# Kernel tuning notes

Hardware: AMD Instinct MI355X
Metric: run time of the kernel (lower is better)

## Reference

```python
import jax, jax.numpy as jnp
import numpy as np

ARITY = 2
DEPTH = 11          # full tree: levels 0..DEPTH, leaves at DEPTH
H = 1024
V = 32001           # vocab_size + 1 (null token)


def _preorder_perm(depth, arity):
    """Permutation mapping pre-order position -> BFS (level-concatenated) index."""
    offsets = np.concatenate([[0], np.cumsum(arity ** np.arange(depth + 1))])
    order = []
    def rec(d, p):
        order.append(int(offsets[d] + p))
        if d < depth:
            for c in range(arity):
                rec(d + 1, p * arity + c)
    rec(0, 0)
    return np.asarray(order, dtype=np.int32)

_PERM = _preorder_perm(DEPTH, ARITY)


def setup_inputs() -> dict:
    key = jax.random.key(0)
    ks = jax.random.split(key, 9)
    s = 0.02  # small init scale for numerical sanity
    return {
        "root_hidden": jax.random.normal(ks[0], (H,), jnp.float32),
        "W1v": jax.random.normal(ks[1], (H, 2 * H), jnp.float32) * s,
        "b1v": jax.random.normal(ks[2], (2 * H,), jnp.float32) * s,
        "W2v": jax.random.normal(ks[3], (2 * H, V), jnp.float32) * s,
        "b2v": jax.random.normal(ks[4], (V,), jnp.float32) * s,
        "W1c": jax.random.normal(ks[5], (H, 2 * H), jnp.float32) * s,
        "b1c": jax.random.normal(ks[6], (2 * H,), jnp.float32) * s,
        "W2c": jax.random.normal(ks[7], (2 * H, ARITY * H), jnp.float32) * s,
        "b2c": jax.random.normal(ks[8], (ARITY * H,), jnp.float32) * s,
    }


def _mlp(h, W1, b1, W2, b2):
    # Linear -> Sigmoid -> Linear (matches nn.Sequential in the torch module)
    return jax.nn.sigmoid(h @ W1 + b1) @ W2 + b2


def reference(root_hidden, W1v, b1v, W2v, b2v, W1c, b1c, W2c, b2c):
    # Level-wise vectorized sweep over the full tree (batches all nodes at a depth).
    h = root_hidden[None, :]                  # [1, H]
    prods = []
    for d in range(DEPTH + 1):
        prods.append(_mlp(h, W1v, b1v, W2v, b2v))     # [a^d, V]
        if d < DEPTH:
            # to_children then split into arity children per node
            h = _mlp(h, W1c, b1c, W2c, b2c).reshape(-1, H)  # [a^(d+1), H]
    raw = jnp.concatenate(prods, axis=0)      # BFS order, [N, V]
    raw = raw[_PERM]                          # reorder to pre-order (torch recursion order)
    return jax.nn.log_softmax(raw, axis=1)
```

## Files before the change

kernel.cpp:

```cpp
#include <hip/hip_runtime.h>
#include <hip/hip_bf16.h>

#define DEPTH_T 11
#define HDIM 1024
#define VDIM 32001
#define NNODES 4095
#define LDV 32008

typedef __attribute__((ext_vector_type(8))) short bf16x8;
typedef __attribute__((ext_vector_type(8))) unsigned short ushort8;
typedef __attribute__((ext_vector_type(4))) float floatx4;

__device__ __forceinline__ int preorder_pos(int m) {
    int q = m + 1;
    int d = 31 - __clz(q);
    int pos = 0;
    for (int i = 1; i <= d; ++i) {
        int b = (q >> (d - i)) & 1;
        pos += 1 + b * ((1 << (DEPTH_T - i + 1)) - 1);
    }
    return pos;
}

__device__ __forceinline__ float bf2f(unsigned short u) {
    return __uint_as_float(((unsigned)u) << 16);
}

#define BM 128
#define BN 128
#define BK 32

template<int MODE, bool SWAPG>
__global__ __launch_bounds__(256, 2) void gemm_bt(
    const __hip_bfloat16* __restrict__ A,
    const __hip_bfloat16* __restrict__ Bt,
    const float* __restrict__ bias,
    void* __restrict__ outp,
    int M, int N, int K, int ldout)
{
    __shared__ __align__(16) __hip_bfloat16 As[BM][BK];
    __shared__ __align__(16) __hip_bfloat16 Bs[BN][BK];

    const int tid  = threadIdx.x;
    const int wave = tid >> 6;
    const int lane = tid & 63;
    const int m0 = (SWAPG ? blockIdx.x : blockIdx.y) * BM;
    const int n0 = (SWAPG ? blockIdx.y : blockIdx.x) * BN;
    const int wm = (wave & 1) * 64;
    const int wn = (wave >> 1) * 64;

    floatx4 acc[4][4];
#pragma unroll
    for (int i = 0; i < 4; ++i)
#pragma unroll
        for (int j = 0; j < 4; ++j) acc[i][j] = (floatx4)0.0f;

    const int lrow = lane >> 2;
    const int lcol = (lane & 3) * 8;
    const int fr = lane & 15;
    const int fk = (lane >> 4) * 8;

    for (int k0 = 0; k0 < K; k0 += BK) {
        __syncthreads();
#pragma unroll
        for (int t = 0; t < 2; ++t) {
            const int r = (wave * 2 + t) * 16;
            int gm = m0 + r + lrow; gm = gm < M ? gm : M - 1;
            const __hip_bfloat16* gp = A + (size_t)gm * K + (k0 + lcol);
            __builtin_amdgcn_global_load_lds(
                (const __attribute__((address_space(1))) void*)gp,
                (__attribute__((address_space(3))) void*)(&As[r][0]),
                16, 0, 0);
        }
#pragma unroll
        for (int t = 0; t < 2; ++t) {
            const int r = (wave * 2 + t) * 16;
            int gn = n0 + r + lrow; gn = gn < N ? gn : N - 1;
            const __hip_bfloat16* gp = Bt + (size_t)gn * K + (k0 + lcol);
            __builtin_amdgcn_global_load_lds(
                (const __attribute__((address_space(1))) void*)gp,
                (__attribute__((address_space(3))) void*)(&Bs[r][0]),
                16, 0, 0);
        }
        __syncthreads();

        bf16x8 af[4], bfv[4];
#pragma unroll
        for (int i = 0; i < 4; ++i)
            af[i] = *(const bf16x8*)(&As[wm + i * 16 + fr][fk]);
#pragma unroll
        for (int j = 0; j < 4; ++j)
            bfv[j] = *(const bf16x8*)(&Bs[wn + j * 16 + fr][fk]);
#pragma unroll
        for (int i = 0; i < 4; ++i)
#pragma unroll
            for (int j = 0; j < 4; ++j)
                acc[i][j] = __builtin_amdgcn_mfma_f32_16x16x32_bf16(
                    af[i], bfv[j], acc[i][j], 0, 0, 0);
    }

    const int rq = (lane >> 4) * 4;
    if (MODE >= 2) {
#pragma unroll
        for (int i = 0; i < 4; ++i) {
#pragma unroll
            for (int r = 0; r < 4; ++r) {
                const int gm = m0 + wm + i * 16 + rq + r;
                if (gm >= M) continue;
                const size_t orow = (size_t)preorder_pos(gm) * ldout;
#pragma unroll
                for (int j = 0; j < 4; ++j) {
                    const int gn = n0 + wn + j * 16 + fr;
                    if (gn < N) {
                        float v = acc[i][j][r] + bias[gn];
                        if (MODE == 2) ((float*)outp)[orow + gn] = v;
                        else ((__hip_bfloat16*)outp)[orow + gn] = __float2bfloat16(v);
                    }
                }
            }
        }
    } else {
        __hip_bfloat16* O = (__hip_bfloat16*)outp;
#pragma unroll
        for (int i = 0; i < 4; ++i) {
#pragma unroll
            for (int r = 0; r < 4; ++r) {
                const int gm = m0 + wm + i * 16 + rq + r;
                if (gm >= M) continue;
#pragma unroll
                for (int j = 0; j < 4; ++j) {
                    const int gn = n0 + wn + j * 16 + fr;
                    if (gn < N) {
                        float v = acc[i][j][r] + bias[gn];
                        if (MODE == 0) v = 1.0f / (1.0f + __expf(-v));
                        O[(size_t)gm * ldout + gn] = __float2bfloat16(v);
                    }
                }
            }
        }
    }
}

#define B2M 256
#define B2N 256

template<int MODE>
__global__ __launch_bounds__(512, 2) void gemm256(
    const __hip_bfloat16* __restrict__ A,
    const __hip_bfloat16* __restrict__ Bt,
    const float* __restrict__ bias,
    void* __restrict__ outp,
    int M, int N, int K, int ldout)
{
    __shared__ __align__(16) char smem[131072];

    const int tid  = threadIdx.x;
    const int wave = tid >> 6;
    const int lane = tid & 63;

    const int nwy = (N + B2N - 1) / B2N;
    int mt, nt;
    {
        const int g = blockIdx.x >> 8;
        const int i = blockIdx.x & 255;
        const int k = i & 7, s = i >> 3;
        mt = (k & 1) * 4 + (s & 3) + (g & 1) * 8;
        nt = (k >> 1) * 8 + (s >> 2) + (g >> 1) * 32;
    }
    if (nt >= nwy) return;
    const int m0 = mt * B2M;
    const int n0 = nt * B2N;

    const int wm = (wave >> 2) * 128;
    const int wn = (wave & 3) * 64;
    const int nkt = K >> 6;

    const int s_row = lane >> 3;
    const int s_col = ((lane & 7) ^ s_row) * 8;

    const int fr  = lane & 15;
    const int fkq = lane >> 4;
    const int swz = (fr & 7) << 4;
    const int c0  = (fkq * 16) ^ swz;
    const int c1  = (64 + fkq * 16) ^ swz;
    const int aoff = (wm + fr) * 128;
    const int boff = 32768 + (wn + fr) * 128;

    floatx4 acc[8][4];
#pragma unroll
    for (int i = 0; i < 8; ++i)
#pragma unroll
        for (int j = 0; j < 4; ++j) acc[i][j] = (floatx4)0.0f;

    bf16x8 a0[8], a1[8], b0[4], b1[4];

    auto mkb = [&](const __hip_bfloat16* gb, int g0, int lim, int h, int inst) {
        int gr = g0 + h * 128 + (inst * 8 + wave) * 8 + s_row;
        gr = gr < lim ? gr : lim - 1;
        return gb + (size_t)gr * K + s_col;
    };
    const __hip_bfloat16* pA00 = mkb(A,  m0, M, 0, 0);
    const __hip_bfloat16* pA01 = mkb(A,  m0, M, 0, 1);
    const __hip_bfloat16* pA10 = mkb(A,  m0, M, 1, 0);
    const __hip_bfloat16* pA11 = mkb(A,  m0, M, 1, 1);
    const __hip_bfloat16* pB00 = mkb(Bt, n0, N, 0, 0);
    const __hip_bfloat16* pB01 = mkb(Bt, n0, N, 0, 1);
    const __hip_bfloat16* pB10 = mkb(Bt, n0, N, 1, 0);
    const __hip_bfloat16* pB11 = mkb(Bt, n0, N, 1, 1);

#define STAGE(bsel, mat, h, PP0, PP1, kt) do { \
    const int ko_ = ((kt) < nkt ? (kt) : 0) * 64; \
    __builtin_amdgcn_global_load_lds( \
        (const __attribute__((address_space(1))) void*)((PP0) + ko_), \
        (__attribute__((address_space(3))) void*) \
            (smem + (bsel)*65536 + (mat)*32768 + (h)*16384 + wave*1024), 16, 0, 0); \
    __builtin_amdgcn_global_load_lds( \
        (const __attribute__((address_space(1))) void*)((PP1) + ko_), \
        (__attribute__((address_space(3))) void*) \
            (smem + (bsel)*65536 + (mat)*32768 + (h)*16384 + 8192 + wave*1024), 16, 0, 0); \
} while (0)

#define RD_A(dst, bsel, cc) \
    _Pragma("unroll") \
    for (int i = 0; i < 8; ++i) \
        dst[i] = *(const bf16x8*)(smem + (bsel) * 65536 + aoff + i * 2048 + (cc));
#define RD_B(dst, bsel, cc) \
    _Pragma("unroll") \
    for (int j = 0; j < 4; ++j) \
        dst[j] = *(const bf16x8*)(smem + (bsel) * 65536 + boff + j * 2048 + (cc));
#define MM(ib, AA, BB) \
    _Pragma("unroll") \
    for (int i = 0; i < 4; ++i) \
    _Pragma("unroll") \
    for (int j = 0; j < 4; ++j) \
        acc[(ib) + i][j] = __builtin_amdgcn_mfma_f32_16x16x32_bf16( \
            AA[(ib) + i], BB[j], acc[(ib) + i][j], 0, 0, 0);
#define LGKM0  asm volatile("s_waitcnt lgkmcnt(0)" ::: "memory")
#define VM4    asm volatile("s_waitcnt vmcnt(4)" ::: "memory")
#define BAR    __builtin_amdgcn_s_barrier()
#define PRIO1  __builtin_amdgcn_s_setprio(1)
#define PRIO0  __builtin_amdgcn_s_setprio(0)

    STAGE(0, 0, 0, pA00, pA01, 0);
    STAGE(0, 0, 1, pA10, pA11, 0);
    STAGE(0, 1, 0, pB00, pB01, 0);
    STAGE(0, 1, 1, pB10, pB11, 0);
    STAGE(1, 0, 0, pA00, pA01, 1);
    STAGE(1, 0, 1, pA10, pA11, 1);
    VM4;
    BAR;

#pragma unroll 1
    for (int t = 0; t < nkt; t += 2) {
        RD_A(a0, 0, c0); RD_B(b0, 0, c0);
        STAGE(1, 1, 0, pB00, pB01, t + 1);
        BAR; LGKM0;
        PRIO1; MM(0, a0, b0); PRIO0;
        BAR;
        RD_A(a1, 0, c1); RD_B(b1, 0, c1);
        STAGE(1, 1, 1, pB10, pB11, t + 1);
        BAR; LGKM0;
        PRIO1; MM(4, a0, b0); PRIO0;
        BAR;
        STAGE(0, 0, 0, pA00, pA01, t + 2);
        BAR;
        PRIO1; MM(0, a1, b1); PRIO0;
        BAR;
        STAGE(0, 0, 1, pA10, pA11, t + 2);
        VM4;
        BAR;
        PRIO1; MM(4, a1, b1); PRIO0;
        BAR;
        RD_A(a0, 1, c0); RD_B(b0, 1, c0);
        STAGE(0, 1, 0, pB00, pB01, t + 2);
        BAR; LGKM0;
        PRIO1; MM(0, a0, b0); PRIO0;
        BAR;
        RD_A(a1, 1, c1); RD_B(b1, 1, c1);
        STAGE(0, 1, 1, pB10, pB11, t + 2);
        BAR; LGKM0;
        PRIO1; MM(4, a0, b0); PRIO0;
        BAR;
        STAGE(1, 0, 0, pA00, pA01, t + 3);
        BAR;
        PRIO1; MM(0, a1, b1); PRIO0;
        BAR;
        STAGE(1, 0, 1, pA10, pA11, t + 3);
        VM4;
        BAR;
        PRIO1; MM(4, a1, b1); PRIO0;
        BAR;
    }

#undef STAGE
#undef RD_A
#undef RD_B
#undef MM
#undef LGKM0
#undef VM4
#undef BAR
#undef PRIO1
#undef PRIO0

    const int rq = (lane >> 4) * 4;
    if (MODE >= 2) {
#pragma unroll
        for (int i = 0; i < 8; ++i) {
#pragma unroll
            for (int r = 0; r < 4; ++r) {
                const int gm = m0 + wm + i * 16 + rq + r;
                if (gm >= M) continue;
                const size_t orow = (size_t)preorder_pos(gm) * ldout;
#pragma unroll
                for (int j = 0; j < 4; ++j) {
                    const int gn = n0 + wn + j * 16 + fr;
                    if (gn < N) {
                        float v = acc[i][j][r] + bias[gn];
                        if (MODE == 2) ((float*)outp)[orow + gn] = v;
                        else ((__hip_bfloat16*)outp)[orow + gn] = __float2bfloat16(v);
                    }
                }
            }
        }
    } else {
        __hip_bfloat16* O = (__hip_bfloat16*)outp;
#pragma unroll
        for (int i = 0; i < 8; ++i) {
#pragma unroll
            for (int r = 0; r < 4; ++r) {
                const int gm = m0 + wm + i * 16 + rq + r;
                if (gm >= M) continue;
#pragma unroll
                for (int j = 0; j < 4; ++j) {
                    const int gn = n0 + wn + j * 16 + fr;
                    if (gn < N) {
                        float v = acc[i][j][r] + bias[gn];
                        if (MODE == 0) v = 1.0f / (1.0f + __expf(-v));
                        O[(size_t)gm * ldout + gn] = __float2bfloat16(v);
                    }
                }
            }
        }
    }
}

template<int MODE>
__global__ __launch_bounds__(256) void gemm_small(
    const __hip_bfloat16* __restrict__ A,
    const __hip_bfloat16* __restrict__ Bt,
    const float* __restrict__ bias,
    __hip_bfloat16* __restrict__ O,
    int M, int N, int K)
{
    const int wave = threadIdx.x >> 6, lane = threadIdx.x & 63;
    const int n0 = blockIdx.x * 64 + wave * 16;
    const int m0 = blockIdx.y * 16;
    const int fr = lane & 15, fk = (lane >> 4) * 8;

    int am = m0 + fr; am = am < M ? am : M - 1;
    const __hip_bfloat16* ap = A + (size_t)am * K + fk;
    const __hip_bfloat16* bp = Bt + (size_t)(n0 + fr) * K + fk;

    floatx4 acc = (floatx4)0.0f;
#pragma unroll 8
    for (int k0 = 0; k0 < K; k0 += 32) {
        bf16x8 av = *(const bf16x8*)(ap + k0);
        bf16x8 bv = *(const bf16x8*)(bp + k0);
        acc = __builtin_amdgcn_mfma_f32_16x16x32_bf16(av, bv, acc, 0, 0, 0);
    }

    const int rq = (lane >> 4) * 4;
    const int gn = n0 + fr;
    const float b = bias[gn];
#pragma unroll
    for (int r = 0; r < 4; ++r) {
        const int gm = m0 + rq + r;
        if (gm >= M) continue;
        float v = acc[r] + b;
        if (MODE == 0) v = 1.0f / (1.0f + __expf(-v));
        O[(size_t)gm * N + gn] = __float2bfloat16(v);
    }
}

__global__ __launch_bounds__(256) void transpose_to_bf16(
    const float* __restrict__ in, __hip_bfloat16* __restrict__ outT, int R, int C)
{
    __shared__ float tile[64][65];
    const int c0 = blockIdx.x * 64, r0 = blockIdx.y * 64;
    const int tx = threadIdx.x & 63, ty = threadIdx.x >> 6;
#pragma unroll
    for (int i = 0; i < 64; i += 4) {
        int r = r0 + ty + i, c = c0 + tx;
        tile[ty + i][tx] = (r < R && c < C) ? in[(size_t)r * C + c] : 0.0f;
    }
    __syncthreads();
#pragma unroll
    for (int i = 0; i < 64; i += 4) {
        int rr = c0 + ty + i, cc = r0 + tx;
        if (rr < C && cc < R) outT[(size_t)rr * R + cc] = __float2bfloat16(tile[tx][ty + i]);
    }
}

__global__ __launch_bounds__(256) void convert_root(
    const float* __restrict__ in, __hip_bfloat16* __restrict__ out)
{
    int i = blockIdx.x * 256 + threadIdx.x;
    if (i < HDIM) out[i] = __float2bfloat16(in[i]);
}

__global__ __launch_bounds__(256) void logsoftmax_bf16(
    const unsigned short* __restrict__ L, float* __restrict__ O)
{
    extern __shared__ char smem[];
    unsigned short* rb = (unsigned short*)smem;
    float* wred = (float*)(smem + 64016);
    const int tid = threadIdx.x, lane = tid & 63, wv = tid >> 6;
    const unsigned short* src = L + (size_t)blockIdx.x * LDV;

    float m = -3.0e38f;
    for (int j = tid * 8; j < 32000; j += 2048) {
        ushort8 u = *(const ushort8*)(src + j);
        *(ushort8*)(rb + j) = u;
#pragma unroll
        for (int t = 0; t < 8; ++t) m = fmaxf(m, bf2f(u[t]));
    }
    if (tid == 0) { unsigned short u = src[32000]; rb[32000] = u; m = fmaxf(m, bf2f(u)); }
#pragma unroll
    for (int off = 32; off; off >>= 1) m = fmaxf(m, __shfl_xor(m, off, 64));
    if (lane == 0) wred[wv] = m;
    __syncthreads();
    const float M4 = fmaxf(fmaxf(wred[0], wred[1]), fmaxf(wred[2], wred[3]));

    float s = 0.0f;
    for (int j = tid * 8; j < 32000; j += 2048) {
        ushort8 u = *(const ushort8*)(rb + j);
#pragma unroll
        for (int t = 0; t < 8; ++t) s += __expf(bf2f(u[t]) - M4);
    }
    if (tid == 0) s += __expf(bf2f(rb[32000]) - M4);
#pragma unroll
    for (int off = 32; off; off >>= 1) s += __shfl_xor(s, off, 64);
    if (lane == 0) wred[4 + wv] = s;
    __syncthreads();
    const float lse = M4 + __logf(wred[4] + wred[5] + wred[6] + wred[7]);

    float* dst = O + (size_t)blockIdx.x * VDIM;
    for (int j = tid * 8; j < 32000; j += 2048) {
        ushort8 u = *(const ushort8*)(rb + j);
#pragma unroll
        for (int t = 0; t < 8; ++t) dst[j + t] = bf2f(u[t]) - lse;
    }
    if (tid == 0) dst[32000] = bf2f(rb[32000]) - lse;
}

__global__ __launch_bounds__(256) void logsoftmax_rows(float* __restrict__ O, int n)
{
    __shared__ float sm[256], ssum[256];
    const int tid = threadIdx.x;
    float* p = O + (size_t)blockIdx.x * n;
    float m = -3.0e38f, s = 0.0f;
    for (int j = tid; j < n; j += 256) {
        float x = p[j];
        float nm = fmaxf(m, x);
        s = s * __expf(m - nm) + __expf(x - nm);
        m = nm;
    }
    sm[tid] = m; ssum[tid] = s;
    __syncthreads();
    for (int off = 128; off > 0; off >>= 1) {
        if (tid < off) {
            float m2 = sm[tid + off], s2 = ssum[tid + off];
            float nm = fmaxf(sm[tid], m2);
            ssum[tid] = ssum[tid] * __expf(sm[tid] - nm) + s2 * __expf(m2 - nm);
            sm[tid] = nm;
        }
        __syncthreads();
    }
    const float lse = sm[0] + __logf(ssum[0]);
    for (int j = tid; j < n; j += 256) p[j] -= lse;
}

extern "C" void kernel_launch(void* const* d_in, const int* in_sizes, int n_in,
                              void* d_out, int out_size, void* d_ws, size_t ws_size,
                              hipStream_t stream)
{
    const float* root = (const float*)d_in[0];
    const float* W1v  = (const float*)d_in[1];
    const float* b1v  = (const float*)d_in[2];
    const float* W2v  = (const float*)d_in[3];
    const float* b2v  = (const float*)d_in[4];
    const float* W1c  = (const float*)d_in[5];
    const float* b1c  = (const float*)d_in[6];
    const float* W2c  = (const float*)d_in[7];
    const float* b2c  = (const float*)d_in[8];

    char* ws = (char*)d_ws;
    __hip_bfloat16* Hall = (__hip_bfloat16*)(ws + 0);
    __hip_bfloat16* X1   = (__hip_bfloat16*)(ws +   8388608ull);
    __hip_bfloat16* Tt   = (__hip_bfloat16*)(ws +  25165824ull);
    __hip_bfloat16* W1vT = (__hip_bfloat16*)(ws +  29360128ull);
    __hip_bfloat16* W1cT = (__hip_bfloat16*)(ws +  33554432ull);
    __hip_bfloat16* W2cT = (__hip_bfloat16*)(ws +  37748736ull);
    __hip_bfloat16* W2vT = (__hip_bfloat16*)(ws +  46137344ull);
    __hip_bfloat16* Lb   = (__hip_bfloat16*)(ws + 177213440ull);
    const bool bf16_logits = ws_size >= 177213440ull + (size_t)NNODES * LDV * 2;

    dim3 blk(256);

    transpose_to_bf16<<<dim3( 32, 16), blk, 0, stream>>>(W1v, W1vT, 1024, 2048);
    transpose_to_bf16<<<dim3(501, 32), blk, 0, stream>>>(W2v, W2vT, 2048, VDIM);
    transpose_to_bf16<<<dim3( 32, 16), blk, 0, stream>>>(W1c, W1cT, 1024, 2048);
    transpose_to_bf16<<<dim3( 32, 32), blk, 0, stream>>>(W2c, W2cT, 2048, 2048);
    convert_root<<<dim3(4), blk, 0, stream>>>(root, Hall);

    for (int d = 0; d < DEPTH_T; ++d) {
        const int Md = 1 << d;
        __hip_bfloat16* Hd = Hall + (size_t)(Md - 1) * HDIM;
        __hip_bfloat16* Hn = Hall + (size_t)((2 << d) - 1) * HDIM;
        if (Md <= 256) {
            dim3 g(32, (Md + 15) / 16);
            gemm_small<0><<<g, blk, 0, stream>>>(Hd, W1cT, b1c, Tt, Md, 2048, 1024);
            gemm_small<1><<<g, blk, 0, stream>>>(Tt, W2cT, b2c, Hn, Md, 2048, 2048);
        } else {
            dim3 g(16, Md / 128);
            gemm_bt<0, false><<<g, blk, 0, stream>>>(Hd, W1cT, b1c, Tt, Md, 2048, 1024, 2048);
            gemm_bt<1, false><<<g, blk, 0, stream>>>(Tt, W2cT, b2c, Hn, Md, 2048, 2048, 2048);
        }
    }

    gemm_bt<0, false><<<dim3(16, 32), blk, 0, stream>>>(Hall, W1vT, b1v, X1, NNODES, 2048, 1024, 2048);
    if (bf16_logits) {
        gemm256<3><<<dim3(2048), dim3(512), 0, stream>>>(X1, W2vT, b2v, Lb, NNODES, VDIM, 2048, LDV);
        logsoftmax_bf16<<<dim3(NNODES), blk, 64048, stream>>>((const unsigned short*)Lb, (float*)d_out);
    } else {
        gemm_bt<2, true><<<dim3(32, 251), blk, 0, stream>>>(X1, W2vT, b2v, d_out, NNODES, VDIM, 2048, VDIM);
        logsoftmax_rows<<<dim3(NNODES), blk, 0, stream>>>((float*)d_out, VDIM);
    }
}
```

Measured before the change: 1.440 ms.

## Run vocab projection GEMM in FP8 e4m3 with FP8 weight transpose and activations

The large vocab GEMM (4095x32001x2048) moves from bf16 MFMA to fp8 e4m3 MFMA. The W2v transpose now writes fp8, and the first vocab MLP layer emits its sigmoid activations directly as fp8. The main kernel's LDS staging is halved and re-swizzled for byte-sized elements, and its register fragments become 64-bit longs. The aim is to double MFMA throughput and halve operand bandwidth for the dominant GEMM, at the cost of much lower precision in the logits, which may break the accuracy tolerance.

After: 1.610 ms. 11.8% more time.

```diff
diff --git a/kernel.cpp b/kernel.cpp
--- a/kernel.cpp
+++ b/kernel.cpp
@@ -24,6 +24,10 @@
 
 __device__ __forceinline__ float bf2f(unsigned short u) {
     return __uint_as_float(((unsigned)u) << 16);
+}
+
+__device__ __forceinline__ unsigned char f2e4m3(float v) {
+    return (unsigned char)(__builtin_amdgcn_cvt_pk_fp8_f32(v, v, 0, false) & 0xff);
 }
 
 #define BM 128
@@ -100,7 +104,7 @@
     }
 
     const int rq = (lane >> 4) * 4;
-    if (MODE >= 2) {
+    if (MODE == 2 || MODE == 3) {
 #pragma unroll
         for (int i = 0; i < 4; ++i) {
 #pragma unroll
@@ -120,7 +124,6 @@
             }
         }
     } else {
-        __hip_bfloat16* O = (__hip_bfloat16*)outp;
 #pragma unroll
         for (int i = 0; i < 4; ++i) {
 #pragma unroll
@@ -132,8 +135,11 @@
                     const int gn = n0 + wn + j * 16 + fr;
                     if (gn < N) {
                         float v = acc[i][j][r] + bias[gn];
-                        if (MODE == 0) v = 1.0f / (1.0f + __expf(-v));
-                        O[(size_t)gm * ldout + gn] = __float2bfloat16(v);
+                        if (MODE != 1) v = 1.0f / (1.0f + __expf(-v));
+                        if (MODE == 4)
+                            ((unsigned char*)outp)[(size_t)gm * ldout + gn] = f2e4m3(v);
+                        else
+                            ((__hip_bfloat16*)outp)[(size_t)gm * ldout + gn] = __float2bfloat16(v);
                     }
                 }
             }
@@ -144,15 +150,14 @@
 #define B2M 256
 #define B2N 256
 
-template<int MODE>
-__global__ __launch_bounds__(512, 2) void gemm256(
-    const __hip_bfloat16* __restrict__ A,
-    const __hip_bfloat16* __restrict__ Bt,
+__global__ __launch_bounds__(512, 1) void gemm256_f8(
+    const unsigned char* __restrict__ A,
+    const unsigned char* __restrict__ Bt,
     const float* __restrict__ bias,
-    void* __restrict__ outp,
+    __hip_bfloat16* __restrict__ outp,
     int M, int N, int K, int ldout)
 {
-    __shared__ __align__(16) char smem[131072];
+    __shared__ __align__(16) char smem[65536];
 
     const int tid  = threadIdx.x;
     const int wave = tid >> 6;
@@ -175,16 +180,16 @@
     const int wn = (wave & 3) * 64;
     const int nkt = K >> 6;
 
-    const int s_row = lane >> 3;
-    const int s_col = ((lane & 7) ^ s_row) * 8;
+    const int s_row = tid >> 2;
+    const int s_col = ((tid & 3) * 16) ^ ((s_row & 3) << 4);
 
     const int fr  = lane & 15;
     const int fkq = lane >> 4;
-    const int swz = (fr & 7) << 4;
-    const int c0  = (fkq * 16) ^ swz;
-    const int c1  = (64 + fkq * 16) ^ swz;
-    const int aoff = (wm + fr) * 128;
-    const int boff = 32768 + (wn + fr) * 128;
+    const int sw  = (fr & 3) << 4;
+    const int c0  = (fkq * 8) ^ sw;
+    const int c1  = (32 + fkq * 8) ^ sw;
+    const int aoff = (wm + fr) * 64;
+    const int boff = 16384 + (wn + fr) * 64;
 
     floatx4 acc[8][4];
 #pragma unroll
@@ -192,152 +197,122 @@
 #pragma unroll
         for (int j = 0; j < 4; ++j) acc[i][j] = (floatx4)0.0f;
 
-    bf16x8 a0[8], a1[8], b0[4], b1[4];
-
-    auto mkb = [&](const __hip_bfloat16* gb, int g0, int lim, int h, int inst) {
-        int gr = g0 + h * 128 + (inst * 8 + wave) * 8 + s_row;
+    long a0[8], a1[8], b0[4], b1[4];
+
+    auto mkb = [&](const unsigned char* gb, int g0, int lim, int h) {
+        int gr = g0 + h * 128 + s_row;
         gr = gr < lim ? gr : lim - 1;
         return gb + (size_t)gr * K + s_col;
     };
-    const __hip_bfloat16* pA00 = mkb(A,  m0, M, 0, 0);
-    const __hip_bfloat16* pA01 = mkb(A,  m0, M, 0, 1);
-    const __hip_bfloat16* pA10 = mkb(A,  m0, M, 1, 0);
-    const __hip_bfloat16* pA11 = mkb(A,  m0, M, 1, 1);
-    const __hip_bfloat16* pB00 = mkb(Bt, n0, N, 0, 0);
-    const __hip_bfloat16* pB01 = mkb(Bt, n0, N, 0, 1);
-    const __hip_bfloat16* pB10 = mkb(Bt, n0, N, 1, 0);
-    const __hip_bfloat16* pB11 = mkb(Bt, n0, N, 1, 1);
-
-#define STAGE(bsel, mat, h, PP0, PP1, kt) do { \
+    const unsigned char* pAlo = mkb(A,  m0, M, 0);
+    const unsigned char* pAhi = mkb(A,  m0, M, 1);
+    const unsigned char* pBlo = mkb(Bt, n0, N, 0);
+    const unsigned char* pBhi = mkb(Bt, n0, N, 1);
+
+#define STAGE8(bsel, mat, h, PP, kt) do { \
     const int ko_ = ((kt) < nkt ? (kt) : 0) * 64; \
     __builtin_amdgcn_global_load_lds( \
-        (const __attribute__((address_space(1))) void*)((PP0) + ko_), \
+        (const __attribute__((address_space(1))) void*)((PP) + ko_), \
         (__attribute__((address_space(3))) void*) \
-            (smem + (bsel)*65536 + (mat)*32768 + (h)*16384 + wave*1024), 16, 0, 0); \
-    __builtin_amdgcn_global_load_lds( \
-        (const __attribute__((address_space(1))) void*)((PP1) + ko_), \
-        (__attribute__((address_space(3))) void*) \
-            (smem + (bsel)*65536 + (mat)*32768 + (h)*16384 + 8192 + wave*1024), 16, 0, 0); \
+            (smem + (bsel)*32768 + (mat)*16384 + (h)*8192 + tid*16), 16, 0, 0); \
 } while (0)
 
-#define RD_A(dst, bsel, cc) \
+#define RD_A8(dst, bsel, cc) \
     _Pragma("unroll") \
     for (int i = 0; i < 8; ++i) \
-        dst[i] = *(const bf16x8*)(smem + (bsel) * 65536 + aoff + i * 2048 + (cc));
-#define RD_B(dst, bsel, cc) \
+        dst[i] = *(const long*)(smem + (bsel) * 32768 + aoff + i * 1024 + (cc));
+#define RD_B8(dst, bsel, cc) \
     _Pragma("unroll") \
     for (int j = 0; j < 4; ++j) \
-        dst[j] = *(const bf16x8*)(smem + (bsel) * 65536 + boff + j * 2048 + (cc));
-#define MM(ib, AA, BB) \
+        dst[j] = *(const long*)(smem + (bsel) * 32768 + boff + j * 1024 + (cc));
+#define MM8(ib, AA, BB) \
     _Pragma("unroll") \
     for (int i = 0; i < 4; ++i) \
     _Pragma("unroll") \
     for (int j = 0; j < 4; ++j) \
-        acc[(ib) + i][j] = __builtin_amdgcn_mfma_f32_16x16x32_bf16( \
+        acc[(ib) + i][j] = __builtin_amdgcn_mfma_f32_16x16x32_fp8_fp8( \
             AA[(ib) + i], BB[j], acc[(ib) + i][j], 0, 0, 0);
 #define LGKM0  asm volatile("s_waitcnt lgkmcnt(0)" ::: "memory")
-#define VM4    asm volatile("s_waitcnt vmcnt(4)" ::: "memory")
+#define VM2    asm volatile("s_waitcnt vmcnt(2)" ::: "memory")
 #define BAR    __builtin_amdgcn_s_barrier()
 #define PRIO1  __builtin_amdgcn_s_setprio(1)
 #define PRIO0  __builtin_amdgcn_s_setprio(0)
 
-    STAGE(0, 0, 0, pA00, pA01, 0);
-    STAGE(0, 0, 1, pA10, pA11, 0);
-    STAGE(0, 1, 0, pB00, pB01, 0);
-    STAGE(0, 1, 1, pB10, pB11, 0);
-    STAGE(1, 0, 0, pA00, pA01, 1);
-    STAGE(1, 0, 1, pA10, pA11, 1);
-    VM4;
+    STAGE8(0, 0, 0, pAlo, 0);
+    STAGE8(0, 0, 1, pAhi, 0);
+    STAGE8(0, 1, 0, pBlo, 0);
+    STAGE8(0, 1, 1, pBhi, 0);
+    STAGE8(1, 0, 0, pAlo, 1);
+    STAGE8(1, 0, 1, pAhi, 1);
+    VM2;
     BAR;
 
 #pragma unroll 1
     for (int t = 0; t < nkt; t += 2) {
-        RD_A(a0, 0, c0); RD_B(b0, 0, c0);
-        STAGE(1, 1, 0, pB00, pB01, t + 1);
+        RD_A8(a0, 0, c0); RD_B8(b0, 0, c0);
+        STAGE8(1, 1, 0, pBlo, t + 1);
         BAR; LGKM0;
-        PRIO1; MM(0, a0, b0); PRIO0;
-        BAR;
-        RD_A(a1, 0, c1); RD_B(b1, 0, c1);
-        STAGE(1, 1, 1, pB10, pB11, t + 1);
+        PRIO1; MM8(0, a0, b0); PRIO0;
+        BAR;
+        RD_A8(a1, 0, c1); RD_B8(b1, 0, c1);
+        STAGE8(1, 1, 1, pBhi, t + 1);
         BAR; LGKM0;
-        PRIO1; MM(4, a0, b0); PRIO0;
-        BAR;
-        STAGE(0, 0, 0, pA00, pA01, t + 2);
-        BAR;
-        PRIO1; MM(0, a1, b1); PRIO0;
-        BAR;
-        STAGE(0, 0, 1, pA10, pA11, t + 2);
-        VM4;
-        BAR;
-        PRIO1; MM(4, a1, b1); PRIO0;
-        BAR;
-        RD_A(a0, 1, c0); RD_B(b0, 1, c0);
-        STAGE(0, 1, 0, pB00, pB01, t + 2);
+        PRIO1; MM8(4, a0, b0); PRIO0;
+        BAR;
+        STAGE8(0, 0, 0, pAlo, t + 2);
+        BAR;
+        PRIO1; MM8(0, a1, b1); PRIO0;
+        BAR;
+        STAGE8(0, 0, 1, pAhi, t + 2);
+        VM2;
+        BAR;
+        PRIO1; MM8(4, a1, b1); PRIO0;
+        BAR;
+        RD_A8(a0, 1, c0); RD_B8(b0, 1, c0);
+        STAGE8(0, 1, 0, pBlo, t + 2);
         BAR; LGKM0;
-        PRIO1; MM(0, a0, b0); PRIO0;
-        BAR;
-        RD_A(a1, 1, c1); RD_B(b1, 1, c1);
-        STAGE(0, 1, 1, pB10, pB11, t + 2);
+        PRIO1; MM8(0, a0, b0); PRIO0;
+        BAR;
+        RD_A8(a1, 1, c1); RD_B8(b1, 1, c1);
+        STAGE8(0, 1, 1, pBhi, t + 2);
         BAR; LGKM0;
-        PRIO1; MM(4, a0, b0); PRIO0;
-        BAR;
-        STAGE(1, 0, 0, pA00, pA01, t + 3);
-        BAR;
-        PRIO1; MM(0, a1, b1); PRIO0;
-        BAR;
-        STAGE(1, 0, 1, pA10, pA11, t + 3);
-        VM4;
-        BAR;
-        PRIO1; MM(4, a1, b1); PRIO0;
-        BAR;
-    }
-
-#undef STAGE
-#undef RD_A
-#undef RD_B
-#undef MM
+        PRIO1; MM8(4, a0, b0); PRIO0;
+        BAR;
+        STAGE8(1, 0, 0, pAlo, t + 3);
+        BAR;
+        PRIO1; MM8(0, a1, b1); PRIO0;
+        BAR;
+        STAGE8(1, 0, 1, pAhi, t + 3);
+        VM2;
+        BAR;
+        PRIO1; MM8(4, a1, b1); PRIO0;
+        BAR;
+    }
+
+#undef STAGE8
+#undef RD_A8
+#undef RD_B8
+#undef MM8
 #undef LGKM0
-#undef VM4
+#undef VM2
 #undef BAR
 #undef PRIO1
 #undef PRIO0
 
     const int rq = (lane >> 4) * 4;
-    if (MODE >= 2) {
-#pragma unroll
-        for (int i = 0; i < 8; ++i) {
-#pragma unroll
-            for (int r = 0; r < 4; ++r) {
-                const int gm = m0 + wm + i * 16 + rq + r;
-                if (gm >= M) continue;
-                const size_t orow = (size_t)preorder_pos(gm) * ldout;
-#pragma unroll
-                for (int j = 0; j < 4; ++j) {
-                    const int gn = n0 + wn + j * 16 + fr;
-                    if (gn < N) {
-                        float v = acc[i][j][r] + bias[gn];
-                        if (MODE == 2) ((float*)outp)[orow + gn] = v;
-                        else ((__hip_bfloat16*)outp)[orow + gn] = __float2bfloat16(v);
-                    }
-                }
-            }
-        }
-    } else {
-        __hip_bfloat16* O = (__hip_bfloat16*)outp;
-#pragma unroll
-        for (int i = 0; i < 8; ++i) {
-#pragma unroll
-            for (int r = 0; r < 4; ++r) {
-                const int gm = m0 + wm + i * 16 + rq + r;
-                if (gm >= M) continue;
-#pragma unroll
-                for (int j = 0; j < 4; ++j) {
-                    const int gn = n0 + wn + j * 16 + fr;
-                    if (gn < N) {
-                        float v = acc[i][j][r] + bias[gn];
-                        if (MODE == 0) v = 1.0f / (1.0f + __expf(-v));
-                        O[(size_t)gm * ldout + gn] = __float2bfloat16(v);
-                    }
+#pragma unroll
+    for (int i = 0; i < 8; ++i) {
+#pragma unroll
+        for (int r = 0; r < 4; ++r) {
+            const int gm = m0 + wm + i * 16 + rq + r;
+            if (gm >= M) continue;
+            const size_t orow = (size_t)preorder_pos(gm) * ldout;
+#pragma unroll
+            for (int j = 0; j < 4; ++j) {
+                const int gn = n0 + wn + j * 16 + fr;
+                if (gn < N) {
+                    float v = acc[i][j][r] + bias[gn];
+                    outp[orow + gn] = __float2bfloat16(v);
                 }
             }
         }
@@ -398,6 +373,25 @@
     for (int i = 0; i < 64; i += 4) {
         int rr = c0 + ty + i, cc = r0 + tx;
         if (rr < C && cc < R) outT[(size_t)rr * R + cc] = __float2bfloat16(tile[tx][ty + i]);
+    }
+}
+
+__global__ __launch_bounds__(256) void transpose_to_fp8(
+    const float* __restrict__ in, unsigned char* __restrict__ outT, int R, int C)
+{
+    __shared__ float tile[64][65];
+    const int c0 = blockIdx.x * 64, r0 = blockIdx.y * 64;
+    const int tx = threadIdx.x & 63, ty = threadIdx.x >> 6;
+#pragma unroll
+    for (int i = 0; i < 64; i += 4) {
+        int r = r0 + ty + i, c = c0 + tx;
+        tile[ty + i][tx] = (r < R && c < C) ? in[(size_t)r * C + c] : 0.0f;
+    }
+    __syncthreads();
+#pragma unroll
+    for (int i = 0; i < 64; i += 4) {
+        int rr = c0 + ty + i, cc = r0 + tx;
+        if (rr < C && cc < R) outT[(size_t)rr * R + cc] = f2e4m3(tile[tx][ty + i]);
     }
 }
 
@@ -497,18 +491,23 @@
     char* ws = (char*)d_ws;
     __hip_bfloat16* Hall = (__hip_bfloat16*)(ws + 0);
     __hip_bfloat16* X1   = (__hip_bfloat16*)(ws +   8388608ull);
+    unsigned char*  X1_8 = (unsigned char*)(ws +   8388608ull);
     __hip_bfloat16* Tt   = (__hip_bfloat16*)(ws +  25165824ull);
     __hip_bfloat16* W1vT = (__hip_bfloat16*)(ws +  29360128ull);
     __hip_bfloat16* W1cT = (__hip_bfloat16*)(ws +  33554432ull);
     __hip_bfloat16* W2cT = (__hip_bfloat16*)(ws +  37748736ull);
     __hip_bfloat16* W2vT = (__hip_bfloat16*)(ws +  46137344ull);
+    unsigned char*  W2vT8= (unsigned char*)(ws +  46137344ull);
     __hip_bfloat16* Lb   = (__hip_bfloat16*)(ws + 177213440ull);
     const bool bf16_logits = ws_size >= 177213440ull + (size_t)NNODES * LDV * 2;
 
     dim3 blk(256);
 
     transpose_to_bf16<<<dim3( 32, 16), blk, 0, stream>>>(W1v, W1vT, 1024, 2048);
-    transpose_to_bf16<<<dim3(501, 32), blk, 0, stream>>>(W2v, W2vT, 2048, VDIM);
+    if (bf16_logits)
+        transpose_to_fp8<<<dim3(501, 32), blk, 0, stream>>>(W2v, W2vT8, 2048, VDIM);
+    else
+        transpose_to_bf16<<<dim3(501, 32), blk, 0, stream>>>(W2v, W2vT, 2048, VDIM);
     transpose_to_bf16<<<dim3( 32, 16), blk, 0, stream>>>(W1c, W1cT, 1024, 2048);
     transpose_to_bf16<<<dim3( 32, 32), blk, 0, stream>>>(W2c, W2cT, 2048, 2048);
     convert_root<<<dim3(4), blk, 0, stream>>>(root, Hall);
@@ -528,11 +527,12 @@
         }
     }
 
-    gemm_bt<0, false><<<dim3(16, 32), blk, 0, stream>>>(Hall, W1vT, b1v, X1, NNODES, 2048, 1024, 2048);
     if (bf16_logits) {
-        gemm256<3><<<dim3(2048), dim3(512), 0, stream>>>(X1, W2vT, b2v, Lb, NNODES, VDIM, 2048, LDV);
+        gemm_bt<4, false><<<dim3(16, 32), blk, 0, stream>>>(Hall, W1vT, b1v, X1_8, NNODES, 2048, 1024, 2048);
+        gemm256_f8<<<dim3(2048), dim3(512), 0, stream>>>(X1_8, W2vT8, b2v, Lb, NNODES, VDIM, 2048, LDV);
         logsoftmax_bf16<<<dim3(NNODES), blk, 64048, stream>>>((const unsigned short*)Lb, (float*)d_out);
     } else {
+        gemm_bt<0, false><<<dim3(16, 32), blk, 0, stream>>>(Hall, W1vT, b1v, X1, NNODES, 2048, 1024, 2048);
         gemm_bt<2, true><<<dim3(32, 251), blk, 0, stream>>>(X1, W2vT, b2v, d_out, NNODES, VDIM, 2048, VDIM);
         logsoftmax_rows<<<dim3(NNODES), blk, 0, stream>>>((float*)d_out, VDIM);
     }
```

## Run vocab projection GEMM in FP8 e4m3 with FP8 MFMA

Applied to the files above, without the earlier changes.

The big logits GEMM (4095x32001x2048) now takes FP8 e4m3 inputs. W2v is transposed straight to FP8, and the sigmoid hidden layer writes FP8 output. The 256x256 kernel is adapted to 128-wide K steps of bytes and issues two fp8 16x16x32 MFMAs per fragment. This halves operand bandwidth and LDS traffic and uses the higher FP8 MFMA throughput, at the cost of lower precision in the logits.

Measured after the change: 1.366 ms. -5.2%, faster.

```diff
diff --git a/kernel.cpp b/kernel.cpp
--- a/kernel.cpp
+++ b/kernel.cpp
@@ -10,6 +10,7 @@
 typedef __attribute__((ext_vector_type(8))) short bf16x8;
 typedef __attribute__((ext_vector_type(8))) unsigned short ushort8;
 typedef __attribute__((ext_vector_type(4))) float floatx4;
+typedef __attribute__((ext_vector_type(2))) long longx2;
 
 __device__ __forceinline__ int preorder_pos(int m) {
     int q = m + 1;
@@ -24,6 +25,10 @@
 
 __device__ __forceinline__ float bf2f(unsigned short u) {
     return __uint_as_float(((unsigned)u) << 16);
+}
+
+__device__ __forceinline__ unsigned char f2e4m3(float v) {
+    return (unsigned char)(__builtin_amdgcn_cvt_pk_fp8_f32(v, v, 0, false) & 0xff);
 }
 
 #define BM 128
@@ -100,7 +105,7 @@
     }
 
     const int rq = (lane >> 4) * 4;
-    if (MODE >= 2) {
+    if (MODE == 2 || MODE == 3) {
 #pragma unroll
         for (int i = 0; i < 4; ++i) {
 #pragma unroll
@@ -120,7 +125,6 @@
             }
         }
     } else {
-        __hip_bfloat16* O = (__hip_bfloat16*)outp;
 #pragma unroll
         for (int i = 0; i < 4; ++i) {
 #pragma unroll
@@ -132,8 +136,11 @@
                     const int gn = n0 + wn + j * 16 + fr;
                     if (gn < N) {
                         float v = acc[i][j][r] + bias[gn];
-                        if (MODE == 0) v = 1.0f / (1.0f + __expf(-v));
-                        O[(size_t)gm * ldout + gn] = __float2bfloat16(v);
+                        if (MODE != 1) v = 1.0f / (1.0f + __expf(-v));
+                        if (MODE == 4)
+                            ((unsigned char*)outp)[(size_t)gm * ldout + gn] = f2e4m3(v);
+                        else
+                            ((__hip_bfloat16*)outp)[(size_t)gm * ldout + gn] = __float2bfloat16(v);
                     }
                 }
             }
@@ -144,12 +151,11 @@
 #define B2M 256
 #define B2N 256
 
-template<int MODE>
-__global__ __launch_bounds__(512, 2) void gemm256(
-    const __hip_bfloat16* __restrict__ A,
-    const __hip_bfloat16* __restrict__ Bt,
+__global__ __launch_bounds__(512, 2) void gemm256_f8(
+    const unsigned char* __restrict__ A,
+    const unsigned char* __restrict__ Bt,
     const float* __restrict__ bias,
-    void* __restrict__ outp,
+    __hip_bfloat16* __restrict__ outp,
     int M, int N, int K, int ldout)
 {
     __shared__ __align__(16) char smem[131072];
@@ -173,10 +179,10 @@
 
     const int wm = (wave >> 2) * 128;
     const int wn = (wave & 3) * 64;
-    const int nkt = K >> 6;
+    const int nkt = K >> 7;
 
     const int s_row = lane >> 3;
-    const int s_col = ((lane & 7) ^ s_row) * 8;
+    const int s_col = ((lane & 7) ^ s_row) * 16;
 
     const int fr  = lane & 15;
     const int fkq = lane >> 4;
@@ -192,24 +198,24 @@
 #pragma unroll
         for (int j = 0; j < 4; ++j) acc[i][j] = (floatx4)0.0f;
 
-    bf16x8 a0[8], a1[8], b0[4], b1[4];
-
-    auto mkb = [&](const __hip_bfloat16* gb, int g0, int lim, int h, int inst) {
+    longx2 a0[8], a1[8], b0[4], b1[4];
+
+    auto mkb = [&](const unsigned char* gb, int g0, int lim, int h, int inst) {
         int gr = g0 + h * 128 + (inst * 8 + wave) * 8 + s_row;
         gr = gr < lim ? gr : lim - 1;
         return gb + (size_t)gr * K + s_col;
     };
-    const __hip_bfloat16* pA00 = mkb(A,  m0, M, 0, 0);
-    const __hip_bfloat16* pA01 = mkb(A,  m0, M, 0, 1);
-    const __hip_bfloat16* pA10 = mkb(A,  m0, M, 1, 0);
-    const __hip_bfloat16* pA11 = mkb(A,  m0, M, 1, 1);
-    const __hip_bfloat16* pB00 = mkb(Bt, n0, N, 0, 0);
-    const __hip_bfloat16* pB01 = mkb(Bt, n0, N, 0, 1);
-    const __hip_bfloat16* pB10 = mkb(Bt, n0, N, 1, 0);
-    const __hip_bfloat16* pB11 = mkb(Bt, n0, N, 1, 1);
+    const unsigned char* pA00 = mkb(A,  m0, M, 0, 0);
+    const unsigned char* pA01 = mkb(A,  m0, M, 0, 1);
+    const unsigned char* pA10 = mkb(A,  m0, M, 1, 0);
+    const unsigned char* pA11 = mkb(A,  m0, M, 1, 1);
+    const unsigned char* pB00 = mkb(Bt, n0, N, 0, 0);
+    const unsigned char* pB01 = mkb(Bt, n0, N, 0, 1);
+    const unsigned char* pB10 = mkb(Bt, n0, N, 1, 0);
+    const unsigned char* pB11 = mkb(Bt, n0, N, 1, 1);
 
 #define STAGE(bsel, mat, h, PP0, PP1, kt) do { \
-    const int ko_ = ((kt) < nkt ? (kt) : 0) * 64; \
+    const int ko_ = ((kt) < nkt ? (kt) : 0) * 128; \
     __builtin_amdgcn_global_load_lds( \
         (const __attribute__((address_space(1))) void*)((PP0) + ko_), \
         (__attribute__((address_space(3))) void*) \
@@ -223,18 +229,21 @@
 #define RD_A(dst, bsel, cc) \
     _Pragma("unroll") \
     for (int i = 0; i < 8; ++i) \
-        dst[i] = *(const bf16x8*)(smem + (bsel) * 65536 + aoff + i * 2048 + (cc));
+        dst[i] = *(const longx2*)(smem + (bsel) * 65536 + aoff + i * 2048 + (cc));
 #define RD_B(dst, bsel, cc) \
     _Pragma("unroll") \
     for (int j = 0; j < 4; ++j) \
-        dst[j] = *(const bf16x8*)(smem + (bsel) * 65536 + boff + j * 2048 + (cc));
+        dst[j] = *(const longx2*)(smem + (bsel) * 65536 + boff + j * 2048 + (cc));
 #define MM(ib, AA, BB) \
     _Pragma("unroll") \
     for (int i = 0; i < 4; ++i) \
     _Pragma("unroll") \
-    for (int j = 0; j < 4; ++j) \
-        acc[(ib) + i][j] = __builtin_amdgcn_mfma_f32_16x16x32_bf16( \
-            AA[(ib) + i], BB[j], acc[(ib) + i][j], 0, 0, 0);
+    for (int j = 0; j < 4; ++j) { \
+        acc[(ib) + i][j] = __builtin_amdgcn_mfma_f32_16x16x32_fp8_fp8( \
+            AA[(ib) + i][0], BB[j][0], acc[(ib) + i][j], 0, 0, 0); \
+        acc[(ib) + i][j] = __builtin_amdgcn_mfma_f32_16x16x32_fp8_fp8( \
+            AA[(ib) + i][1], BB[j][1], acc[(ib) + i][j], 0, 0, 0); \
+    }
 #define LGKM0  asm volatile("s_waitcnt lgkmcnt(0)" ::: "memory")
 #define VM4    asm volatile("s_waitcnt vmcnt(4)" ::: "memory")
 #define BAR    __builtin_amdgcn_s_barrier()
@@ -303,41 +312,19 @@
 #undef PRIO0
 
     const int rq = (lane >> 4) * 4;
-    if (MODE >= 2) {
-#pragma unroll
-        for (int i = 0; i < 8; ++i) {
-#pragma unroll
-            for (int r = 0; r < 4; ++r) {
-                const int gm = m0 + wm + i * 16 + rq + r;
-                if (gm >= M) continue;
-                const size_t orow = (size_t)preorder_pos(gm) * ldout;
-#pragma unroll
-                for (int j = 0; j < 4; ++j) {
-                    const int gn = n0 + wn + j * 16 + fr;
-                    if (gn < N) {
-                        float v = acc[i][j][r] + bias[gn];
-                        if (MODE == 2) ((float*)outp)[orow + gn] = v;
-                        else ((__hip_bfloat16*)outp)[orow + gn] = __float2bfloat16(v);
-                    }
-                }
-            }
-        }
-    } else {
-        __hip_bfloat16* O = (__hip_bfloat16*)outp;
-#pragma unroll
-        for (int i = 0; i < 8; ++i) {
-#pragma unroll
-            for (int r = 0; r < 4; ++r) {
-                const int gm = m0 + wm + i * 16 + rq + r;
-                if (gm >= M) continue;
-#pragma unroll
-                for (int j = 0; j < 4; ++j) {
-                    const int gn = n0 + wn + j * 16 + fr;
-                    if (gn < N) {
-                        float v = acc[i][j][r] + bias[gn];
-                        if (MODE == 0) v = 1.0f / (1.0f + __expf(-v));
-                        O[(size_t)gm * ldout + gn] = __float2bfloat16(v);
-                    }
+#pragma unroll
+    for (int i = 0; i < 8; ++i) {
+#pragma unroll
+        for (int r = 0; r < 4; ++r) {
+            const int gm = m0 + wm + i * 16 + rq + r;
+            if (gm >= M) continue;
+            const size_t orow = (size_t)preorder_pos(gm) * ldout;
+#pragma unroll
+            for (int j = 0; j < 4; ++j) {
+                const int gn = n0 + wn + j * 16 + fr;
+                if (gn < N) {
+                    float v = acc[i][j][r] + bias[gn];
+                    outp[orow + gn] = __float2bfloat16(v);
                 }
             }
         }
@@ -398,6 +385,25 @@
     for (int i = 0; i < 64; i += 4) {
         int rr = c0 + ty + i, cc = r0 + tx;
         if (rr < C && cc < R) outT[(size_t)rr * R + cc] = __float2bfloat16(tile[tx][ty + i]);
+    }
+}
+
+__global__ __launch_bounds__(256) void transpose_to_fp8(
+    const float* __restrict__ in, unsigned char* __restrict__ outT, int R, int C)
+{
+    __shared__ float tile[64][65];
+    const int c0 = blockIdx.x * 64, r0 = blockIdx.y * 64;
+    const int tx = threadIdx.x & 63, ty = threadIdx.x >> 6;
+#pragma unroll
+    for (int i = 0; i < 64; i += 4) {
+        int r = r0 + ty + i, c = c0 + tx;
+        tile[ty + i][tx] = (r < R && c < C) ? in[(size_t)r * C + c] : 0.0f;
+    }
+    __syncthreads();
+#pragma unroll
+    for (int i = 0; i < 64; i += 4) {
+        int rr = c0 + ty + i, cc = r0 + tx;
+        if (rr < C && cc < R) outT[(size_t)rr * R + cc] = f2e4m3(tile[tx][ty + i]);
     }
 }
 
@@ -497,18 +503,23 @@
     char* ws = (char*)d_ws;
     __hip_bfloat16* Hall = (__hip_bfloat16*)(ws + 0);
     __hip_bfloat16* X1   = (__hip_bfloat16*)(ws +   8388608ull);
+    unsigned char*  X1_8 = (unsigned char*)(ws +   8388608ull);
     __hip_bfloat16* Tt   = (__hip_bfloat16*)(ws +  25165824ull);
     __hip_bfloat16* W1vT = (__hip_bfloat16*)(ws +  29360128ull);
     __hip_bfloat16* W1cT = (__hip_bfloat16*)(ws +  33554432ull);
     __hip_bfloat16* W2cT = (__hip_bfloat16*)(ws +  37748736ull);
     __hip_bfloat16* W2vT = (__hip_bfloat16*)(ws +  46137344ull);
+    unsigned char*  W2vT8= (unsigned char*)(ws +  46137344ull);
     __hip_bfloat16* Lb   = (__hip_bfloat16*)(ws + 177213440ull);
     const bool bf16_logits = ws_size >= 177213440ull + (size_t)NNODES * LDV * 2;
 
     dim3 blk(256);
 
     transpose_to_bf16<<<dim3( 32, 16), blk, 0, stream>>>(W1v, W1vT, 1024, 2048);
-    transpose_to_bf16<<<dim3(501, 32), blk, 0, stream>>>(W2v, W2vT, 2048, VDIM);
+    if (bf16_logits)
+        transpose_to_fp8<<<dim3(501, 32), blk, 0, stream>>>(W2v, W2vT8, 2048, VDIM);
+    else
+        transpose_to_bf16<<<dim3(501, 32), blk, 0, stream>>>(W2v, W2vT, 2048, VDIM);
     transpose_to_bf16<<<dim3( 32, 16), blk, 0, stream>>>(W1c, W1cT, 1024, 2048);
     transpose_to_bf16<<<dim3( 32, 32), blk, 0, stream>>>(W2c, W2cT, 2048, 2048);
     convert_root<<<dim3(4), blk, 0, stream>>>(root, Hall);
@@ -528,11 +539,12 @@
         }
     }
 
-    gemm_bt<0, false><<<dim3(16, 32), blk, 0, stream>>>(Hall, W1vT, b1v, X1, NNODES, 2048, 1024, 2048);
     if (bf16_logits) {
-        gemm256<3><<<dim3(2048), dim3(512), 0, stream>>>(X1, W2vT, b2v, Lb, NNODES, VDIM, 2048, LDV);
+        gemm_bt<4, false><<<dim3(16, 32), blk, 0, stream>>>(Hall, W1vT, b1v, X1_8, NNODES, 2048, 1024, 2048);
+        gemm256_f8<<<dim3(2048), dim3(512), 0, stream>>>(X1_8, W2vT8, b2v, Lb, NNODES, VDIM, 2048, LDV);
         logsoftmax_bf16<<<dim3(NNODES), blk, 64048, stream>>>((const unsigned short*)Lb, (float*)d_out);
     } else {
+        gemm_bt<0, false><<<dim3(16, 32), blk, 0, stream>>>(Hall, W1vT, b1v, X1, NNODES, 2048, 1024, 2048);
         gemm_bt<2, true><<<dim3(32, 251), blk, 0, stream>>>(X1, W2vT, b2v, d_out, NNODES, VDIM, 2048, VDIM);
         logsoftmax_rows<<<dim3(NNODES), blk, 0, stream>>>((float*)d_out, VDIM);
     }
```
